# Kernel tuning notes

Measured on AMD Instinct MI355X. Metric: run time of the kernel, lower is better.

## Reference

```python
import jax, jax.numpy as jnp
import numpy as np

MARGIN = 0.1
EPS = 1e-6  # torch CosineSimilarity eps


def setup_inputs() -> dict:
    key = jax.random.key(0)
    k1, k2 = jax.random.split(key)
    pred = jax.random.normal(k1, (8192, 512), dtype=jnp.float32)
    labels = jax.random.randint(k2, (8192,), 0, 14)  # one-hot gt <=> int labels
    return {"pred": pred, "labels": labels}


def _cosine(x, y):
    # torch.nn.CosineSimilarity(dim=1, eps=1e-6): clamp norms at eps
    nx = jnp.maximum(jnp.linalg.norm(x, axis=1), EPS)
    ny = jnp.maximum(jnp.linalg.norm(y, axis=1), EPS)
    return jnp.sum(x * y, axis=1) / (nx * ny)


def reference(pred, labels):
    B = pred.shape[0]
    # rows_pos: rows sharing the anchor's label (includes anchor itself, as in torch code)
    pos_mask = labels[:, None] == labels[None, :]  # [B, B] bool
    # random.sample(rows, 1) -> uniform random valid index per row, via gumbel-argmax
    kp, kn = jax.random.split(jax.random.key(42))
    neg_inf = jnp.float32(-1e30)
    g_pos = jax.random.gumbel(kp, (B, B), dtype=jnp.float32)
    g_neg = jax.random.gumbel(kn, (B, B), dtype=jnp.float32)
    idx_p = jnp.argmax(jnp.where(pos_mask, g_pos, neg_inf), axis=1)  # [B]
    idx_n = jnp.argmax(jnp.where(pos_mask, neg_inf, g_neg), axis=1)  # [B]

    anchor = pred
    positive = pred[idx_p]
    negative = pred[idx_n]
    cos_v = _cosine(anchor, positive) - _cosine(anchor, negative) + MARGIN
    return jnp.mean(jnp.maximum(cos_v, 0.0))
```

## Files before the change

### kernel.cpp

```cpp
#include <hip/hip_runtime.h>
#include <stdint.h>


#define B_ROWS 8192
#define DIMS   512
#define NLAB   16

__device__ __forceinline__ uint32_t rotl(uint32_t x, uint32_t r) {
  return __builtin_amdgcn_alignbit(x, x, 32u - r);
}

struct KeyPair { uint32_t a, b; };
constexpr KeyPair tf_c(uint32_t k0, uint32_t k1, uint32_t x0, uint32_t x1) {
  const uint32_t ks2 = k0 ^ k1 ^ 0x1BD11BDAu;
  x0 += k0; x1 += k1;
#define TFRC(r) { x0 += x1; x1 = (uint32_t)((x1 << (r)) | (x1 >> (32 - (r)))); x1 ^= x0; }
  TFRC(13) TFRC(15) TFRC(26) TFRC(6)
  x0 += k1;  x1 += ks2 + 1u;
  TFRC(17) TFRC(29) TFRC(16) TFRC(24)
  x0 += ks2; x1 += k0 + 2u;
  TFRC(13) TFRC(15) TFRC(26) TFRC(6)
  x0 += k0;  x1 += k1 + 3u;
  TFRC(17) TFRC(29) TFRC(16) TFRC(24)
  x0 += k1;  x1 += ks2 + 4u;
  TFRC(13) TFRC(15) TFRC(26) TFRC(6)
  x0 += ks2; x1 += k0 + 5u;
#undef TFRC
  return {x0, x1};
}
constexpr KeyPair KP = tf_c(0u, 42u, 0u, 0u);
constexpr KeyPair KN = tf_c(0u, 42u, 0u, 1u);

template <uint32_t K0, uint32_t K1>
__device__ __forceinline__ uint32_t tf_draw(uint32_t x1) {
  constexpr uint32_t KS2 = K0 ^ K1 ^ 0x1BD11BDAu;
  uint32_t x0 = K0;
#define TFR(r) { x0 += x1; x1 = rotl(x1, r); x1 ^= x0; }
  TFR(13) TFR(15) TFR(26) TFR(6)
  x0 += K1;  x1 += KS2 + 1u;
  TFR(17) TFR(29) TFR(16) TFR(24)
  x0 += KS2; x1 += K0 + 2u;
  TFR(13) TFR(15) TFR(26) TFR(6)
  x0 += K0;  x1 += K1 + 3u;
  TFR(17) TFR(29) TFR(16) TFR(24)
  x0 += K1;  x1 += KS2 + 4u;
  TFR(13) TFR(15) TFR(26) TFR(6)
  x0 += KS2; x1 += K0 + 5u;
#undef TFR
  return x0 ^ x1;
}

__global__ __launch_bounds__(256) void sort_kernel(const int* __restrict__ labels,
                                                   int* __restrict__ perm,
                                                   int* __restrict__ gstart) {
  __shared__ int cnt[NLAB][256];
  __shared__ int gs[NLAB + 1];
  const int t = threadIdx.x;
  for (int l = 0; l < NLAB; ++l) cnt[l][t] = 0;
  __syncthreads();
  const int base = t * 32;
  for (int e = base; e < base + 32; ++e) cnt[labels[e]][t]++;
  __syncthreads();
  if (t < NLAB) {
    int run = 0;
    for (int k = 0; k < 256; ++k) { const int c = cnt[t][k]; cnt[t][k] = run; run += c; }
    gs[t + 1] = run;
  }
  __syncthreads();
  if (t == 0) {
    gs[0] = 0;
    for (int l = 1; l <= NLAB; ++l) gs[l] += gs[l - 1];
  }
  __syncthreads();
  for (int e = base; e < base + 32; ++e) {
    const int l = labels[e];
    perm[gs[l] + cnt[l][t]++] = e;
  }
  if (t <= NLAB) gstart[t] = gs[t];
}

__global__ __launch_bounds__(256) void norms_kernel(const float* __restrict__ pred,
                                                    float* __restrict__ norms) {
  const int wave = threadIdx.x >> 6, lane = threadIdx.x & 63;
  const int r = blockIdx.x * 4 + wave;
  const float4* A = (const float4*)(pred + (size_t)r * DIMS);
  float s = 0.f;
#pragma unroll
  for (int t = 0; t < 2; ++t) {
    const float4 a = A[lane + 64 * t];
    s += a.x * a.x + a.y * a.y + a.z * a.z + a.w * a.w;
  }
  for (int o = 32; o > 0; o >>= 1) s += __shfl_down(s, o, 64);
  if (lane == 0) norms[r] = sqrtf(s);
}

__global__ __launch_bounds__(256) void argmax_kernel(const int* __restrict__ labels,
                                                     const int* __restrict__ perm,
                                                     const int* __restrict__ gstart,
                                                     int* __restrict__ idxp,
                                                     int* __restrict__ idxn) {
  const int lane = threadIdx.x & 63;
  const int r = blockIdx.x * 4 + (threadIdx.x >> 6);
  const int li = __builtin_amdgcn_readfirstlane(labels[r]);
  const int g0 = __builtin_amdgcn_readfirstlane(gstart[li]);
  const int g1 = __builtin_amdgcn_readfirstlane(gstart[li + 1]);
  const uint32_t base = (uint32_t)r << 13;

  int bv = -1, bi = 0;
  const uint32_t sbp = base + KP.b;
  for (int t = g0 + lane; t < g1; t += 64) {
    const int j = perm[t];
    const uint32_t w = tf_draw<KP.a, KP.b>(sbp + (uint32_t)j);
    const int v = (int)(w >> 9);
    const bool better = (v > bv) || ((v == bv) && (j < bi));
    bv = better ? v : bv;
    bi = better ? j : bi;
  }
  unsigned long long pp =
      (((unsigned long long)(bv + 1)) << 13) | (unsigned)(8191 - bi);

  bv = -1; bi = 0;
  const int glen = g1 - g0;
  const int nneg = B_ROWS - glen;
  const uint32_t sbn = base + KN.b;
#pragma unroll 2
  for (int t = lane; t < nneg; t += 64) {
    const int tj = (t < g0) ? t : (t + glen);
    const int j = perm[tj];
    const uint32_t w = tf_draw<KN.a, KN.b>(sbn + (uint32_t)j);
    const int v = (int)(w >> 9);
    const bool better = (v > bv) || ((v == bv) && (j < bi));
    bv = better ? v : bv;
    bi = better ? j : bi;
  }
  unsigned long long pn =
      (((unsigned long long)(bv + 1)) << 13) | (unsigned)(8191 - bi);

  for (int o = 32; o > 0; o >>= 1) {
    const unsigned long long t1 = __shfl_down(pp, o, 64); if (t1 > pp) pp = t1;
    const unsigned long long t2 = __shfl_down(pn, o, 64); if (t2 > pn) pn = t2;
  }
  if (lane == 0) {
    idxp[r] = 8191 - (int)(pp & 8191ull);
    idxn[r] = 8191 - (int)(pn & 8191ull);
  }
}

__global__ __launch_bounds__(256) void cos_kernel(const float* __restrict__ pred,
                                                  const float* __restrict__ norms,
                                                  const int* __restrict__ idxp,
                                                  const int* __restrict__ idxn,
                                                  float* __restrict__ cosv) {
  const int wave = threadIdx.x >> 6, lane = threadIdx.x & 63;
  const int r = blockIdx.x * 4 + wave;
  const int ip = idxp[r], inn = idxn[r];
  const float4* A = (const float4*)(pred + (size_t)r * DIMS);
  const float4* P = (const float4*)(pred + (size_t)ip * DIMS);
  const float4* Nn = (const float4*)(pred + (size_t)inn * DIMS);
  float dp = 0.f, dn = 0.f;
#pragma unroll
  for (int t = 0; t < 2; ++t) {
    const float4 a = A[lane + 64 * t];
    const float4 p = P[lane + 64 * t];
    const float4 n = Nn[lane + 64 * t];
    dp += a.x * p.x + a.y * p.y + a.z * p.z + a.w * p.w;
    dn += a.x * n.x + a.y * n.y + a.z * n.z + a.w * n.w;
  }
  for (int o = 32; o > 0; o >>= 1) {
    dp += __shfl_down(dp, o, 64);
    dn += __shfl_down(dn, o, 64);
  }
  if (lane == 0) {
    const float na = fmaxf(norms[r], 1e-6f);
    const float np = fmaxf(norms[ip], 1e-6f);
    const float nn = fmaxf(norms[inn], 1e-6f);
    const float c = dp / (na * np) - dn / (na * nn) + 0.1f;
    cosv[r] = fmaxf(c, 0.f);
  }
}

__global__ __launch_bounds__(256) void reduce_kernel(const float* __restrict__ cosv,
                                                     float* __restrict__ out) {
  __shared__ double sh[4];
  double s = 0.0;
  for (int j = threadIdx.x; j < B_ROWS; j += 256) s += (double)cosv[j];
  for (int o = 32; o > 0; o >>= 1) s += __shfl_down(s, o, 64);
  const int wave = threadIdx.x >> 6, lane = threadIdx.x & 63;
  if (lane == 0) sh[wave] = s;
  __syncthreads();
  if (threadIdx.x == 0) {
    const double t = sh[0] + sh[1] + sh[2] + sh[3];
    out[0] = (float)(t / (double)B_ROWS);
  }
}

extern "C" void kernel_launch(void* const* d_in, const int* in_sizes, int n_in,
                              void* d_out, int out_size, void* d_ws, size_t ws_size,
                              hipStream_t stream) {
  const float* pred  = (const float*)d_in[0];
  const int* labels  = (const int*)d_in[1];
  float* out = (float*)d_out;

  char* ws = (char*)d_ws;
  float* norms  = (float*)(ws + 0);
  int*   idxp   = (int*)(ws + 32 * 1024);
  int*   idxn   = (int*)(ws + 64 * 1024);
  float* cosv   = (float*)(ws + 96 * 1024);
  int*   perm   = (int*)(ws + 128 * 1024);
  int*   gstart = (int*)(ws + 160 * 1024);

  sort_kernel<<<1, 256, 0, stream>>>(labels, perm, gstart);
  norms_kernel<<<B_ROWS / 4, 256, 0, stream>>>(pred, norms);
  argmax_kernel<<<B_ROWS / 4, 256, 0, stream>>>(labels, perm, gstart, idxp, idxn);
  cos_kernel<<<B_ROWS / 4, 256, 0, stream>>>(pred, norms, idxp, idxn, cosv);
  reduce_kernel<<<1, 256, 0, stream>>>(cosv, out);
}
```

Before: 229.0 us.

## Unroll argmax loops 4-way with prefetched perm indices and simplified threefry

Rewrites the argmax scan so each lane handles four independent candidates per iteration, keeping four running maxima that are merged at the end. The next batch of perm indices is prefetched before the current batch is hashed, so load latency overlaps with the threefry work. The threefry routine is also rewritten with key additions folded into fewer instructions. The cost is more registers, plus clamped out-of-range loads and masked tail lanes.

```diff
diff --git a/kernel.cpp b/kernel.cpp
--- a/kernel.cpp
+++ b/kernel.cpp
@@ -34,20 +34,32 @@
 template <uint32_t K0, uint32_t K1>
 __device__ __forceinline__ uint32_t tf_draw(uint32_t x1) {
   constexpr uint32_t KS2 = K0 ^ K1 ^ 0x1BD11BDAu;
-  uint32_t x0 = K0;
-#define TFR(r) { x0 += x1; x1 = rotl(x1, r); x1 ^= x0; }
-  TFR(13) TFR(15) TFR(26) TFR(6)
-  x0 += K1;  x1 += KS2 + 1u;
-  TFR(17) TFR(29) TFR(16) TFR(24)
-  x0 += KS2; x1 += K0 + 2u;
-  TFR(13) TFR(15) TFR(26) TFR(6)
-  x0 += K0;  x1 += K1 + 3u;
-  TFR(17) TFR(29) TFR(16) TFR(24)
-  x0 += K1;  x1 += KS2 + 4u;
-  TFR(13) TFR(15) TFR(26) TFR(6)
-  x0 += KS2; x1 += K0 + 5u;
-#undef TFR
-  return x0 ^ x1;
+  uint32_t x0 = K0 + x1;
+  x1 = rotl(x1, 13); x1 ^= x0;
+  x0 += x1; x1 = rotl(x1, 15); x1 ^= x0;
+  x0 += x1; x1 = rotl(x1, 26); x1 ^= x0;
+  x0 += x1; x1 = rotl(x1, 6);  x1 ^= x0;
+  x1 += KS2 + 1u;  x0 = x0 + x1 + K1;
+  x1 = rotl(x1, 17); x1 ^= x0;
+  x0 += x1; x1 = rotl(x1, 29); x1 ^= x0;
+  x0 += x1; x1 = rotl(x1, 16); x1 ^= x0;
+  x0 += x1; x1 = rotl(x1, 24); x1 ^= x0;
+  x1 += K0 + 2u;   x0 = x0 + x1 + KS2;
+  x1 = rotl(x1, 13); x1 ^= x0;
+  x0 += x1; x1 = rotl(x1, 15); x1 ^= x0;
+  x0 += x1; x1 = rotl(x1, 26); x1 ^= x0;
+  x0 += x1; x1 = rotl(x1, 6);  x1 ^= x0;
+  x1 += K1 + 3u;   x0 = x0 + x1 + K0;
+  x1 = rotl(x1, 17); x1 ^= x0;
+  x0 += x1; x1 = rotl(x1, 29); x1 ^= x0;
+  x0 += x1; x1 = rotl(x1, 16); x1 ^= x0;
+  x0 += x1; x1 = rotl(x1, 24); x1 ^= x0;
+  x1 += KS2 + 4u;  x0 = x0 + x1 + K1;
+  x1 = rotl(x1, 13); x1 ^= x0;
+  x0 += x1; x1 = rotl(x1, 15); x1 ^= x0;
+  x0 += x1; x1 = rotl(x1, 26); x1 ^= x0;
+  x0 += x1; x1 = rotl(x1, 6);  x1 ^= x0;
+  return (x0 + KS2) ^ (x1 + K0 + 5u);
 }
 
 __global__ __launch_bounds__(256) void sort_kernel(const int* __restrict__ labels,
@@ -104,37 +116,93 @@
   const int li = __builtin_amdgcn_readfirstlane(labels[r]);
   const int g0 = __builtin_amdgcn_readfirstlane(gstart[li]);
   const int g1 = __builtin_amdgcn_readfirstlane(gstart[li + 1]);
+  const int glen = g1 - g0;
   const uint32_t base = (uint32_t)r << 13;
 
-  int bv = -1, bi = 0;
-  const uint32_t sbp = base + KP.b;
-  for (int t = g0 + lane; t < g1; t += 64) {
-    const int j = perm[t];
-    const uint32_t w = tf_draw<KP.a, KP.b>(sbp + (uint32_t)j);
-    const int v = (int)(w >> 9);
-    const bool better = (v > bv) || ((v == bv) && (j < bi));
-    bv = better ? v : bv;
-    bi = better ? j : bi;
-  }
-  unsigned long long pp =
-      (((unsigned long long)(bv + 1)) << 13) | (unsigned)(8191 - bi);
-
-  bv = -1; bi = 0;
-  const int glen = g1 - g0;
-  const int nneg = B_ROWS - glen;
-  const uint32_t sbn = base + KN.b;
-#pragma unroll 2
-  for (int t = lane; t < nneg; t += 64) {
-    const int tj = (t < g0) ? t : (t + glen);
-    const int j = perm[tj];
-    const uint32_t w = tf_draw<KN.a, KN.b>(sbn + (uint32_t)j);
-    const int v = (int)(w >> 9);
-    const bool better = (v > bv) || ((v == bv) && (j < bi));
-    bv = better ? v : bv;
-    bi = better ? j : bi;
-  }
-  unsigned long long pn =
-      (((unsigned long long)(bv + 1)) << 13) | (unsigned)(8191 - bi);
+  unsigned long long pp, pn;
+
+  {
+    const uint32_t sb = base + KP.b;
+    const int niter = (glen + 255) >> 8;
+    int bv[4] = {-1, -1, -1, -1}, bi[4] = {0, 0, 0, 0};
+    int j[4], jn[4];
+    int tb = g0 + lane;
+#pragma unroll
+    for (int c = 0; c < 4; ++c) jn[c] = perm[min(tb + 64 * c, 8191)];
+    for (int it = 0; it < niter; ++it) {
+#pragma unroll
+      for (int c = 0; c < 4; ++c) j[c] = jn[c];
+      const int tbn = tb + 256;
+#pragma unroll
+      for (int c = 0; c < 4; ++c) jn[c] = perm[min(tbn + 64 * c, 8191)];
+#pragma unroll
+      for (int c = 0; c < 4; ++c) {
+        const uint32_t w = tf_draw<KP.a, KP.b>(sb + (uint32_t)j[c]);
+        const int t = tb + 64 * c;
+        const int v = (t < g1) ? (int)(w >> 9) : -1;
+        const bool better =
+            (v > bv[c]) || ((v == bv[c]) && ((unsigned)j[c] < (unsigned)bi[c]));
+        bv[c] = better ? v : bv[c];
+        bi[c] = better ? j[c] : bi[c];
+      }
+      tb = tbn;
+    }
+    int BV = bv[0], BI = bi[0];
+#pragma unroll
+    for (int c = 1; c < 4; ++c) {
+      const bool better =
+          (bv[c] > BV) || ((bv[c] == BV) && ((unsigned)bi[c] < (unsigned)BI));
+      BV = better ? bv[c] : BV;
+      BI = better ? bi[c] : BI;
+    }
+    pp = (((unsigned long long)(BV + 1)) << 13) | (unsigned)(8191 - BI);
+  }
+
+  {
+    const uint32_t sb = base + KN.b;
+    const int nneg = B_ROWS - glen;
+    const int niter = (nneg + 255) >> 8;
+    int bv[4] = {-1, -1, -1, -1}, bi[4] = {0, 0, 0, 0};
+    int j[4], jn[4];
+    int tb = lane;
+#pragma unroll
+    for (int c = 0; c < 4; ++c) {
+      const int t = tb + 64 * c;
+      const int tj = (t < g0) ? t : t + glen;
+      jn[c] = perm[min(tj, 8191)];
+    }
+    for (int it = 0; it < niter; ++it) {
+#pragma unroll
+      for (int c = 0; c < 4; ++c) j[c] = jn[c];
+      const int tbn = tb + 256;
+#pragma unroll
+      for (int c = 0; c < 4; ++c) {
+        const int t = tbn + 64 * c;
+        const int tj = (t < g0) ? t : t + glen;
+        jn[c] = perm[min(tj, 8191)];
+      }
+#pragma unroll
+      for (int c = 0; c < 4; ++c) {
+        const uint32_t w = tf_draw<KN.a, KN.b>(sb + (uint32_t)j[c]);
+        const int t = tb + 64 * c;
+        const int v = (t < nneg) ? (int)(w >> 9) : -1;
+        const bool better =
+            (v > bv[c]) || ((v == bv[c]) && ((unsigned)j[c] < (unsigned)bi[c]));
+        bv[c] = better ? v : bv[c];
+        bi[c] = better ? j[c] : bi[c];
+      }
+      tb = tbn;
+    }
+    int BV = bv[0], BI = bi[0];
+#pragma unroll
+    for (int c = 1; c < 4; ++c) {
+      const bool better =
+          (bv[c] > BV) || ((bv[c] == BV) && ((unsigned)bi[c] < (unsigned)BI));
+      BV = better ? bv[c] : BV;
+      BI = better ? bi[c] : BI;
+    }
+    pn = (((unsigned long long)(BV + 1)) << 13) | (unsigned)(8191 - BI);
+  }
 
   for (int o = 32; o > 0; o >>= 1) {
     const unsigned long long t1 = __shfl_down(pp, o, 64); if (t1 > pp) pp = t1;
```

Result: slower. 234.9 us (+2.6%).

## Fuse sort into norms kernel and scan negatives via packed shared-memory labels

Applied to the files above, without the earlier changes.

Merges the single-block label sort into the norms kernel, with block 0 doing the sort after its norm work, which removes one launch. The argmax kernel now stages all labels as packed bytes in shared memory. The negative scan then walks every index j in order, masking out same-label rows, instead of gathering through perm, which gives contiguous counters and an unrolled loop of 8. The threefry rounds are reordered to fold the key adds, and the tie-break compare is dropped because in-order traversal already keeps the first maximum. The cost is that every argmax block loads the full 32KB label array into LDS, and the negative loop always runs over all 8192 entries.

```diff
diff --git a/kernel.cpp b/kernel.cpp
--- a/kernel.cpp
+++ b/kernel.cpp
@@ -34,27 +34,54 @@
 template <uint32_t K0, uint32_t K1>
 __device__ __forceinline__ uint32_t tf_draw(uint32_t x1) {
   constexpr uint32_t KS2 = K0 ^ K1 ^ 0x1BD11BDAu;
-  uint32_t x0 = K0;
-#define TFR(r) { x0 += x1; x1 = rotl(x1, r); x1 ^= x0; }
-  TFR(13) TFR(15) TFR(26) TFR(6)
-  x0 += K1;  x1 += KS2 + 1u;
-  TFR(17) TFR(29) TFR(16) TFR(24)
-  x0 += KS2; x1 += K0 + 2u;
-  TFR(13) TFR(15) TFR(26) TFR(6)
-  x0 += K0;  x1 += K1 + 3u;
-  TFR(17) TFR(29) TFR(16) TFR(24)
-  x0 += K1;  x1 += KS2 + 4u;
-  TFR(13) TFR(15) TFR(26) TFR(6)
-  x0 += KS2; x1 += K0 + 5u;
-#undef TFR
-  return x0 ^ x1;
-}
-
-__global__ __launch_bounds__(256) void sort_kernel(const int* __restrict__ labels,
-                                                   int* __restrict__ perm,
-                                                   int* __restrict__ gstart) {
+  uint32_t x0 = K0 + x1;
+  x1 = rotl(x1, 13); x1 ^= x0;
+  x0 += x1; x1 = rotl(x1, 15); x1 ^= x0;
+  x0 += x1; x1 = rotl(x1, 26); x1 ^= x0;
+  x0 += x1; x1 = rotl(x1, 6);  x1 ^= x0;
+  x1 += KS2 + 1u;  x0 = x0 + x1 + K1;
+  x1 = rotl(x1, 17); x1 ^= x0;
+  x0 += x1; x1 = rotl(x1, 29); x1 ^= x0;
+  x0 += x1; x1 = rotl(x1, 16); x1 ^= x0;
+  x0 += x1; x1 = rotl(x1, 24); x1 ^= x0;
+  x1 += K0 + 2u;   x0 = x0 + x1 + KS2;
+  x1 = rotl(x1, 13); x1 ^= x0;
+  x0 += x1; x1 = rotl(x1, 15); x1 ^= x0;
+  x0 += x1; x1 = rotl(x1, 26); x1 ^= x0;
+  x0 += x1; x1 = rotl(x1, 6);  x1 ^= x0;
+  x1 += K1 + 3u;   x0 = x0 + x1 + K0;
+  x1 = rotl(x1, 17); x1 ^= x0;
+  x0 += x1; x1 = rotl(x1, 29); x1 ^= x0;
+  x0 += x1; x1 = rotl(x1, 16); x1 ^= x0;
+  x0 += x1; x1 = rotl(x1, 24); x1 ^= x0;
+  x1 += KS2 + 4u;  x0 = x0 + x1 + K1;
+  x1 = rotl(x1, 13); x1 ^= x0;
+  x0 += x1; x1 = rotl(x1, 15); x1 ^= x0;
+  x0 += x1; x1 = rotl(x1, 26); x1 ^= x0;
+  x0 += x1; x1 = rotl(x1, 6);  x1 ^= x0;
+  return (x0 + KS2) ^ (x1 + K0 + 5u);
+}
+
+__global__ __launch_bounds__(256) void norms_sort_kernel(const float* __restrict__ pred,
+                                                         const int* __restrict__ labels,
+                                                         float* __restrict__ norms,
+                                                         int* __restrict__ perm,
+                                                         int* __restrict__ gstart) {
   __shared__ int cnt[NLAB][256];
   __shared__ int gs[NLAB + 1];
+  const int wave = threadIdx.x >> 6, lane = threadIdx.x & 63;
+  const int r = blockIdx.x * 4 + wave;
+  const float4* A = (const float4*)(pred + (size_t)r * DIMS);
+  float s = 0.f;
+#pragma unroll
+  for (int t = 0; t < 2; ++t) {
+    const float4 a = A[lane + 64 * t];
+    s += a.x * a.x + a.y * a.y + a.z * a.z + a.w * a.w;
+  }
+  for (int o = 32; o > 0; o >>= 1) s += __shfl_down(s, o, 64);
+  if (lane == 0) norms[r] = sqrtf(s);
+
+  if (blockIdx.x != 0) return;
   const int t = threadIdx.x;
   for (int l = 0; l < NLAB; ++l) cnt[l][t] = 0;
   __syncthreads();
@@ -77,21 +104,6 @@
     perm[gs[l] + cnt[l][t]++] = e;
   }
   if (t <= NLAB) gstart[t] = gs[t];
-}
-
-__global__ __launch_bounds__(256) void norms_kernel(const float* __restrict__ pred,
-                                                    float* __restrict__ norms) {
-  const int wave = threadIdx.x >> 6, lane = threadIdx.x & 63;
-  const int r = blockIdx.x * 4 + wave;
-  const float4* A = (const float4*)(pred + (size_t)r * DIMS);
-  float s = 0.f;
-#pragma unroll
-  for (int t = 0; t < 2; ++t) {
-    const float4 a = A[lane + 64 * t];
-    s += a.x * a.x + a.y * a.y + a.z * a.z + a.w * a.w;
-  }
-  for (int o = 32; o > 0; o >>= 1) s += __shfl_down(s, o, 64);
-  if (lane == 0) norms[r] = sqrtf(s);
 }
 
 __global__ __launch_bounds__(256) void argmax_kernel(const int* __restrict__ labels,
@@ -99,42 +111,62 @@
                                                      const int* __restrict__ gstart,
                                                      int* __restrict__ idxp,
                                                      int* __restrict__ idxn) {
-  const int lane = threadIdx.x & 63;
-  const int r = blockIdx.x * 4 + (threadIdx.x >> 6);
+  __shared__ uint32_t labw[B_ROWS / 4];
+  const int tid = threadIdx.x;
+  {
+    const int4* L4 = (const int4*)labels;
+#pragma unroll
+    for (int q = 0; q < 8; ++q) {
+      const int4 a = L4[tid * 8 + q];
+      labw[tid * 8 + q] = (uint32_t)a.x | ((uint32_t)a.y << 8) |
+                          ((uint32_t)a.z << 16) | ((uint32_t)a.w << 24);
+    }
+  }
+  const int lane = tid & 63;
+  const int r = blockIdx.x * 4 + (tid >> 6);
   const int li = __builtin_amdgcn_readfirstlane(labels[r]);
   const int g0 = __builtin_amdgcn_readfirstlane(gstart[li]);
   const int g1 = __builtin_amdgcn_readfirstlane(gstart[li + 1]);
   const uint32_t base = (uint32_t)r << 13;
 
-  int bv = -1, bi = 0;
-  const uint32_t sbp = base + KP.b;
-  for (int t = g0 + lane; t < g1; t += 64) {
-    const int j = perm[t];
-    const uint32_t w = tf_draw<KP.a, KP.b>(sbp + (uint32_t)j);
-    const int v = (int)(w >> 9);
-    const bool better = (v > bv) || ((v == bv) && (j < bi));
-    bv = better ? v : bv;
-    bi = better ? j : bi;
+  int bv = -1, bj = 0;
+  {
+    const uint32_t sb = base + KP.b;
+    for (int t = g0 + lane; t < g1; t += 64) {
+      const int j = perm[t];
+      const uint32_t w = tf_draw<KP.a, KP.b>(sb + (uint32_t)j);
+      const int v = (int)(w >> 9);
+      const bool upd = v > bv;
+      bv = upd ? v : bv;
+      bj = upd ? j : bj;
+    }
   }
   unsigned long long pp =
-      (((unsigned long long)(bv + 1)) << 13) | (unsigned)(8191 - bi);
-
-  bv = -1; bi = 0;
-  const int glen = g1 - g0;
-  const int nneg = B_ROWS - glen;
-  const uint32_t sbn = base + KN.b;
-#pragma unroll 2
-  for (int t = lane; t < nneg; t += 64) {
-    const int tj = (t < g0) ? t : (t + glen);
-    const int j = perm[tj];
-    const uint32_t w = tf_draw<KN.a, KN.b>(sbn + (uint32_t)j);
-    const int v = (int)(w >> 9);
-    const bool better = (v > bv) || ((v == bv) && (j < bi));
-    bv = better ? v : bv;
-    bi = better ? j : bi;
+      (((unsigned long long)(bv + 1)) << 13) | (unsigned)(8191 - bj);
+
+  __syncthreads();
+
+  bv = -1; bj = 0;
+  {
+    const uint8_t* lb = (const uint8_t*)labw;
+    uint32_t x1w = base + KN.b + (uint32_t)lane;
+    int jw = lane;
+#pragma unroll 1
+    for (int it = 0; it < 128; it += 8) {
+#pragma unroll
+      for (int u = 0; u < 8; ++u) {
+        const uint32_t w = tf_draw<KN.a, KN.b>(x1w + 64u * u);
+        const int lab = (int)lb[jw + 64 * u];
+        const int v = (int)(w >> 9);
+        const bool upd = (lab != li) & (v > bv);
+        bv = upd ? v : bv;
+        bj = upd ? (jw + 64 * u) : bj;
+      }
+      x1w += 512u; jw += 512;
+    }
   }
   unsigned long long pn =
-      (((unsigned long long)(bv + 1)) << 13) | (unsigned)(8191 - bi);
+      (((unsigned long long)(bv + 1)) << 13) | (unsigned)(8191 - bj);
 
   for (int o = 32; o > 0; o >>= 1) {
     const unsigned long long t1 = __shfl_down(pp, o, 64); if (t1 > pp) pp = t1;
@@ -209,8 +241,7 @@
   int*   perm   = (int*)(ws + 128 * 1024);
   int*   gstart = (int*)(ws + 160 * 1024);
 
-  sort_kernel<<<1, 256, 0, stream>>>(labels, perm, gstart);
-  norms_kernel<<<B_ROWS / 4, 256, 0, stream>>>(pred, norms);
+  norms_sort_kernel<<<B_ROWS / 4, 256, 0, stream>>>(pred, labels, norms, perm, gstart);
   argmax_kernel<<<B_ROWS / 4, 256, 0, stream>>>(labels, perm, gstart, idxp, idxn);
   cos_kernel<<<B_ROWS / 4, 256, 0, stream>>>(pred, norms, idxp, idxn, cosv);
   reduce_kernel<<<1, 256, 0, stream>>>(cosv, out);
```

Result: slower. 260.1 us (+13.6%).
